# Kernel optimization log

Measured on AMD Instinct MI355X. Metric: run time of the kernel, lower is better.

Reference implementation:

```python
import jax, jax.numpy as jnp
import numpy as np
import math

B, S, D, H = 2, 2048, 1024, 16
DH = D // H  # head_dim = 64


def setup_inputs() -> dict:
    key = jax.random.key(0)
    k0, k1, k2 = jax.random.split(key, 3)
    x = jax.random.normal(k0, (B, S, D), dtype=jnp.float32)
    Wi = jax.random.normal(k1, (3 * D, D), dtype=jnp.float32) * 0.02  # torch (out,in) layout
    bi = jnp.zeros((3 * D,), dtype=jnp.float32)
    Wo = jax.random.normal(k2, (D, D), dtype=jnp.float32) * 0.02
    bo = jnp.zeros((D,), dtype=jnp.float32)
    return {"x": x, "Wi": Wi, "bi": bi, "Wo": Wo, "bo": bo, "causal_mask": 1}


def reference(x, Wi, bi, Wo, bo, causal_mask):
    b, s, d = x.shape
    # fused QKV projection: nn.Linear applies x @ W.T + b
    qkv = x @ Wi.T + bi                      # (b, s, 3d)
    q, k, v = jnp.split(qkv, 3, axis=-1)
    # (b, s, d) -> (b, h, s, dh)
    def to_heads(t):
        return t.reshape(b, s, H, DH).transpose(0, 2, 1, 3)
    q, k, v = to_heads(q), to_heads(k), to_heads(v)
    scores = jnp.einsum("bhqd,bhkd->bhqk", q, k)  # (b, h, s, s)
    if causal_mask:
        # mask strictly-upper triangle with -inf BEFORE scaling (as in source; -inf unaffected)
        tri = jnp.triu(jnp.ones((s, s), dtype=bool), k=1)
        scores = jnp.where(tri, -jnp.inf, scores)
    scores = scores / math.sqrt(DH)
    weight = jax.nn.softmax(scores, axis=-1)
    out = jnp.einsum("bhqk,bhkd->bhqd", weight, v)  # (b, h, s, dh)
    out = out.transpose(0, 2, 1, 3).reshape(b, s, d)
    return out @ Wo.T + bo
```

## Files before the change

kernel.cpp:

```cpp
#include <hip/hip_runtime.h>
#include <hip/hip_bf16.h>
#include <stdint.h>

#define B_    2
#define S_    2048
#define D_    1024
#define H_    16
#define DH_   64
#define MTOT  (B_*S_)
#define NQKV  (3*D_)

typedef __attribute__((ext_vector_type(8))) short  bf16x8;
typedef __attribute__((ext_vector_type(4))) short  bf16x4;
typedef __attribute__((ext_vector_type(4))) float  f32x4;
typedef __attribute__((ext_vector_type(8))) unsigned short u16x8;
typedef unsigned short ushort_t;

__device__ __forceinline__ ushort_t f2bf(float f) {
  union { float f; unsigned int i; } v; v.f = f;
  unsigned int r = v.i + 0x7FFF + ((v.i >> 16) & 1);
  return (ushort_t)(r >> 16);
}

__device__ __forceinline__ unsigned cvt_pk_bf16(float lo, float hi) {
  unsigned r;
  asm("v_cvt_pk_bf16_f32 %0, %1, %2" : "=v"(r) : "v"(lo), "v"(hi));
  return r;
}

__device__ __forceinline__ float fexp2(float x) {
  float r;
  asm("v_exp_f32 %0, %1" : "=v"(r) : "v"(x));
  return r;
}

#if __has_builtin(__builtin_amdgcn_mfma_f32_16x16x16_bf16)
__device__ __forceinline__ f32x4 mfma16(bf16x4 a, bf16x4 b, f32x4 c) {
  return __builtin_amdgcn_mfma_f32_16x16x16_bf16(a, b, c, 0, 0, 0);
}
#elif __has_builtin(__builtin_amdgcn_mfma_f32_16x16x16bf16_1k)
__device__ __forceinline__ f32x4 mfma16(bf16x4 a, bf16x4 b, f32x4 c) {
  return __builtin_amdgcn_mfma_f32_16x16x16bf16_1k(a, b, c, 0, 0, 0);
}
#else
__device__ __forceinline__ f32x4 mfma16(bf16x4 a, bf16x4 b, f32x4 c) {
  asm volatile("v_mfma_f32_16x16x16_bf16 %0, %1, %2, %0"
               : "+v"(c) : "v"(a), "v"(b));
  return c;
}
#endif

__device__ __forceinline__ void gl_lds16(const ushort_t* g, ushort_t* l) {
  __builtin_amdgcn_global_load_lds(
      (const __attribute__((address_space(1))) unsigned int*)g,
      (__attribute__((address_space(3))) unsigned int*)l, 16, 0, 0);
}

#define CVN1 (MTOT*D_/8)
#define CVN2 (NQKV*D_/8)
#define CVN3 (D_*D_/8)
__global__ __launch_bounds__(256) void cvt_all(
    const float* __restrict__ x, const float* __restrict__ Wi, const float* __restrict__ Wo,
    ushort_t* __restrict__ xb, ushort_t* __restrict__ Wib, ushort_t* __restrict__ Wob) {
  int i = blockIdx.x * blockDim.x + threadIdx.x;
  const float* src; ushort_t* dst; int k;
  if (i < CVN1)            { src = x;  dst = xb;  k = i; }
  else if (i < CVN1+CVN2)  { src = Wi; dst = Wib; k = i - CVN1; }
  else                     { src = Wo; dst = Wob; k = i - CVN1 - CVN2; }
  const float4* s4 = (const float4*)src;
  float4 a = s4[2*k], b = s4[2*k+1];
  u16x8 o;
  o[0]=f2bf(a.x); o[1]=f2bf(a.y); o[2]=f2bf(a.z); o[3]=f2bf(a.w);
  o[4]=f2bf(b.x); o[5]=f2bf(b.y); o[6]=f2bf(b.z); o[7]=f2bf(b.w);
  ((u16x8*)dst)[k] = o;
}

#define BKg 32
#define QSCALE 0.18033688011112042f
__global__ __launch_bounds__(256) void gemm_qkv(
    const ushort_t* __restrict__ Abf, const ushort_t* __restrict__ Bbf,
    const float* __restrict__ bias,
    ushort_t* __restrict__ qb, ushort_t* __restrict__ kb, ushort_t* __restrict__ vb) {
  __shared__ __align__(16) ushort_t Al[2][128*BKg];
  __shared__ __align__(16) ushort_t Bl[2][128*BKg];
  int tid = threadIdx.x;
  int w = tid >> 6, lane = tid & 63;
  int wrow = (w >> 1) * 64, wcol = (w & 1) * 64;
  int m0 = blockIdx.y * 128, n0 = blockIdx.x * 128;
  const int K = D_;
  const int nt = K / BKg;

  auto stageg = [&](int t, int buf) {
    int k0 = t * BKg;
    #pragma unroll
    for (int it = 0; it < 2; ++it) {
      int c = it*256 + tid;
      int row = c >> 2, cc = c & 3;
      int lbase = (it*256 + w*64) * 8;
      gl_lds16(Abf + (size_t)(m0+row)*K + k0 + cc*8, &Al[buf][lbase]);
      gl_lds16(Bbf + (size_t)(n0+row)*K + k0 + cc*8, &Bl[buf][lbase]);
    }
  };

  f32x4 zero = {0.f, 0.f, 0.f, 0.f};
  f32x4 acc[4][4];
  for (int i=0;i<4;i++) for (int j=0;j<4;j++) acc[i][j] = zero;

  stageg(0, 0);
  __syncthreads();

  for (int t = 0; t < nt; ++t) {
    int cur = t & 1;
    if (t + 1 < nt) stageg(t + 1, cur ^ 1);
    int kof = (lane >> 4) * 8;
    bf16x8 af[4], bfr[4];
    for (int i=0;i<4;i++) af[i]  = *(const bf16x8*)(&Al[cur][(wrow + i*16 + (lane&15))*BKg + kof]);
    for (int j=0;j<4;j++) bfr[j] = *(const bf16x8*)(&Bl[cur][(wcol + j*16 + (lane&15))*BKg + kof]);
    for (int i=0;i<4;i++)
      for (int j=0;j<4;j++)
        acc[i][j] = __builtin_amdgcn_mfma_f32_16x16x32_bf16(af[i], bfr[j], acc[i][j], 0, 0, 0);
    __syncthreads();
  }
  for (int i=0;i<4;i++)
    for (int j=0;j<4;j++)
      for (int r=0;r<4;r++) {
        int gm = m0 + wrow + i*16 + (lane>>4)*4 + r;
        int gn = n0 + wcol + j*16 + (lane&15);
        float v = acc[i][j][r] + bias[gn];
        int b = gm >> 11, s = gm & (S_-1);
        int sect = gn >> 10, hn = gn & (D_-1);
        int hh = hn >> 6, d = hn & 63;
        size_t idx = (((size_t)(b*H_ + hh))*S_ + s)*DH_ + d;
        if (sect == 0) v *= QSCALE;
        ushort_t val = f2bf(v);
        if (sect == 0) qb[idx] = val;
        else if (sect == 1) kb[idx] = val;
        else vb[idx] = val;
      }
}

__global__ __launch_bounds__(256) void transpose_v(
    const ushort_t* __restrict__ vb, ushort_t* __restrict__ vtb) {
  __shared__ ushort_t T[64*72];
  int bh = blockIdx.y;
  int s0 = blockIdx.x * 64;
  int tid = threadIdx.x;
  const ushort_t* src = vb + (size_t)bh * S_ * DH_;
  ushort_t* dst = vtb + (size_t)bh * DH_ * S_;
  for (int it = 0; it < 2; ++it) {
    int c = it*256 + tid;
    int row = c >> 3, cc = c & 7;
    *(uint4*)&T[row*72 + cc*8] = *(const uint4*)(src + (size_t)(s0+row)*DH_ + cc*8);
  }
  __syncthreads();
  for (int it = 0; it < 2; ++it) {
    int c = it*256 + tid;
    int d = c >> 3, sc = c & 7;
    u16x8 o;
    #pragma unroll
    for (int e = 0; e < 8; ++e) o[e] = T[(sc*8+e)*72 + d];
    *(u16x8*)(dst + (size_t)d*S_ + s0 + sc*8) = o;
  }
}

#define KVB 64
#define DTHR 8.0f
__global__ __launch_bounds__(256) void attn_fwd(
    const ushort_t* __restrict__ qb, const ushort_t* __restrict__ kb,
    const ushort_t* __restrict__ vtb, ushort_t* __restrict__ attnb,
    const int* __restrict__ causal) {
  int wg = blockIdx.x;
  int xcd = wg & 7;
  int rest = wg >> 3;
  int bh = (rest & 3) * 8 + xcd;
  int qblk = 31 - (rest >> 2);
  int b = bh >> 4, h = bh & 15;
  int tid = threadIdx.x, w = tid >> 6, lane = tid & 63;
  int g = lane >> 4, q16 = lane & 15;
  const ushort_t* qh  = qb  + (size_t)bh * S_ * DH_;
  const ushort_t* kh  = kb  + (size_t)bh * S_ * DH_;
  const ushort_t* vth = vtb + (size_t)bh * DH_ * S_;
  __shared__ __align__(16) ushort_t Kl[3][KVB*64];
  __shared__ __align__(16) ushort_t Vtl[3][64*KVB];
  bool use_causal = (causal[0] != 0);

  int nkv = use_causal ? (qblk + 1) : (S_/KVB);
  int qw = qblk*64 + w*16;

  bf16x8 qc0 = *(const bf16x8*)(qh + (size_t)(qw + q16)*DH_ +  0 + g*8);
  bf16x8 qc1 = *(const bf16x8*)(qh + (size_t)(qw + q16)*DH_ + 32 + g*8);

  int c0 = tid, c1 = tid + 256;
  int r0 = c0 >> 3, sw0 = ((c0 & 7) ^ (r0 & 7)) * 8;
  int r1 = c1 >> 3, sw1 = ((c1 & 7) ^ (r1 & 7)) * 8;
  const ushort_t* kp0 = kh + r0*DH_ + sw0;
  const ushort_t* kp1 = kh + r1*DH_ + sw1;
  const ushort_t* vp0 = vth + (size_t)r0*S_ + sw0;
  const ushort_t* vp1 = vth + (size_t)r1*S_ + sw1;

  auto stage = [&](int t, int buf) {
    size_t kadv = (size_t)(t*KVB) * DH_;
    int vadv = t*KVB;
    gl_lds16(kp0 + kadv, &Kl[buf][c0*8]);
    gl_lds16(kp1 + kadv, &Kl[buf][c1*8]);
    gl_lds16(vp0 + vadv, &Vtl[buf][c0*8]);
    gl_lds16(vp1 + vadv, &Vtl[buf][c1*8]);
  };

  f32x4 zero = {0.f,0.f,0.f,0.f};
  f32x4 o[4];
  #pragma unroll
  for (int dt=0;dt<4;dt++) o[dt] = zero;
  float mrun = -1e30f, lrun = 0.f;

  stage(0, 0);
  stage(1, 1);
  asm volatile("s_waitcnt vmcnt(4)" ::: "memory");
  __builtin_amdgcn_s_barrier();

  for (int it = 0; it < nkv; ++it) {
    int cur = it % 3;
    int kvbase = it * KVB;
    if (it + 2 < nkv) stage(it + 2, (it + 2) % 3);

    f32x4 sacc[4];
    #pragma unroll
    for (int j=0;j<4;j++) sacc[j] = zero;
    #pragma unroll
    for (int kk=0;kk<2;kk++) {
      bf16x8 qf = kk ? qc1 : qc0;
      #pragma unroll
      for (int j=0;j<4;j++) {
        int row = j*16 + q16;
        int slot = (kk*4 + g) ^ (row & 7);
        bf16x8 kf = *(const bf16x8*)(&Kl[cur][row*64 + slot*8]);
        sacc[j] = __builtin_amdgcn_mfma_f32_16x16x32_bf16(kf, qf, sacc[j], 0, 0, 0);
      }
    }
    if (use_causal && kvbase + KVB - 1 > qw) {
      int qd = qw + q16 - kvbase;
      #pragma unroll
      for (int j=0;j<4;j++)
        #pragma unroll
        for (int r=0;r<4;r++)
          if (16*j + 4*g + r > qd) sacc[j][r] = -1e30f;
    }
    float m0v = fmaxf(fmaxf(sacc[0][0], sacc[0][1]), fmaxf(sacc[0][2], sacc[0][3]));
    float m1v = fmaxf(fmaxf(sacc[1][0], sacc[1][1]), fmaxf(sacc[1][2], sacc[1][3]));
    float m2v = fmaxf(fmaxf(sacc[2][0], sacc[2][1]), fmaxf(sacc[2][2], sacc[2][3]));
    float m3v = fmaxf(fmaxf(sacc[3][0], sacc[3][1]), fmaxf(sacc[3][2], sacc[3][3]));
    float mx = fmaxf(fmaxf(m0v, m1v), fmaxf(m2v, m3v));
    mx = fmaxf(mx, __shfl_xor(mx, 16, 64));
    mx = fmaxf(mx, __shfl_xor(mx, 32, 64));
    if (!__all(mx - mrun <= DTHR)) {
      float mnew = fmaxf(mrun, mx);
      float alpha = fexp2(mrun - mnew);
      lrun *= alpha;
      float av0 = __shfl(alpha, 4*g + 0, 64);
      float av1 = __shfl(alpha, 4*g + 1, 64);
      float av2 = __shfl(alpha, 4*g + 2, 64);
      float av3 = __shfl(alpha, 4*g + 3, 64);
      #pragma unroll
      for (int dt=0;dt<4;dt++) {
        o[dt][0] *= av0; o[dt][1] *= av1; o[dt][2] *= av2; o[dt][3] *= av3;
      }
      mrun = mnew;
    }
    float p[4][4];
    float rs = 0.f;
    #pragma unroll
    for (int j=0;j<4;j++)
      #pragma unroll
      for (int r=0;r<4;r++) {
        p[j][r] = fexp2(sacc[j][r] - mrun);
        rs += p[j][r];
      }
    rs += __shfl_xor(rs, 16, 64);
    rs += __shfl_xor(rs, 32, 64);
    lrun += rs;
    #pragma unroll
    for (int s=0;s<4;s++) {
      union { unsigned u[2]; bf16x4 v; } pk;
      pk.u[0] = cvt_pk_bf16(p[s][0], p[s][1]);
      pk.u[1] = cvt_pk_bf16(p[s][2], p[s][3]);
      int E = 16*s + 4*g;
      #pragma unroll
      for (int dt=0;dt<4;dt++) {
        int row = dt*16 + q16;
        int off = row*64 + ((E >> 3) ^ (row & 7))*8 + (E & 7);
        bf16x4 vf = *(const bf16x4*)(&Vtl[cur][off]);
        o[dt] = mfma16(pk.v, vf, o[dt]);
      }
    }
    if (it + 2 < nkv) {
      asm volatile("s_waitcnt vmcnt(4)" ::: "memory");
    } else {
      asm volatile("s_waitcnt vmcnt(0)" ::: "memory");
    }
    __builtin_amdgcn_s_barrier();
  }
  float li0 = 1.f / __shfl(lrun, 4*g + 0, 64);
  float li1 = 1.f / __shfl(lrun, 4*g + 1, 64);
  float li2 = 1.f / __shfl(lrun, 4*g + 2, 64);
  float li3 = 1.f / __shfl(lrun, 4*g + 3, 64);
  #pragma unroll
  for (int r=0;r<4;r++) {
    float li = (r==0)?li0:(r==1)?li1:(r==2)?li2:li3;
    int q = qw + 4*g + r;
    #pragma unroll
    for (int dt=0;dt<4;dt++) {
      int d = dt*16 + q16;
      attnb[((size_t)(b*S_ + q))*D_ + h*DH_ + d] = f2bf(o[dt][r] * li);
    }
  }
}

__global__ __launch_bounds__(256) void gemm_out(
    const ushort_t* __restrict__ Abf, const ushort_t* __restrict__ Bbf,
    const float* __restrict__ bias, float* __restrict__ out) {
  __shared__ __align__(16) ushort_t Al[2][128*BKg];
  __shared__ __align__(16) ushort_t Bl[2][128*BKg];
  int tid = threadIdx.x;
  int w = tid >> 6, lane = tid & 63;
  int wrow = (w >> 1) * 64, wcol = (w & 1) * 64;
  int m0 = blockIdx.y * 128, n0 = blockIdx.x * 128;
  const int K = D_;
  const int nt = K / BKg;

  auto stageg = [&](int t, int buf) {
    int k0 = t * BKg;
    #pragma unroll
    for (int it = 0; it < 2; ++it) {
      int c = it*256 + tid;
      int row = c >> 2, cc = c & 3;
      int lbase = (it*256 + w*64) * 8;
      gl_lds16(Abf + (size_t)(m0+row)*K + k0 + cc*8, &Al[buf][lbase]);
      gl_lds16(Bbf + (size_t)(n0+row)*K + k0 + cc*8, &Bl[buf][lbase]);
    }
  };

  f32x4 zero = {0.f,0.f,0.f,0.f};
  f32x4 acc[4][4];
  for (int i=0;i<4;i++) for (int j=0;j<4;j++) acc[i][j] = zero;

  stageg(0, 0);
  __syncthreads();

  for (int t = 0; t < nt; ++t) {
    int cur = t & 1;
    if (t + 1 < nt) stageg(t + 1, cur ^ 1);
    int kof = (lane >> 4) * 8;
    bf16x8 af[4], bfr[4];
    for (int i=0;i<4;i++) af[i]  = *(const bf16x8*)(&Al[cur][(wrow + i*16 + (lane&15))*BKg + kof]);
    for (int j=0;j<4;j++) bfr[j] = *(const bf16x8*)(&Bl[cur][(wcol + j*16 + (lane&15))*BKg + kof]);
    for (int i=0;i<4;i++)
      for (int j=0;j<4;j++)
        acc[i][j] = __builtin_amdgcn_mfma_f32_16x16x32_bf16(af[i], bfr[j], acc[i][j], 0, 0, 0);
    __syncthreads();
  }
  for (int i=0;i<4;i++)
    for (int j=0;j<4;j++)
      for (int r=0;r<4;r++) {
        int gm = m0 + wrow + i*16 + (lane>>4)*4 + r;
        int gn = n0 + wcol + j*16 + (lane&15);
        out[(size_t)gm*D_ + gn] = acc[i][j][r] + bias[gn];
      }
}

extern "C" void kernel_launch(void* const* d_in, const int* in_sizes, int n_in,
                              void* d_out, int out_size, void* d_ws, size_t ws_size,
                              hipStream_t stream) {
  const float* x  = (const float*)d_in[0];
  const float* Wi = (const float*)d_in[1];
  const float* bi = (const float*)d_in[2];
  const float* Wo = (const float*)d_in[3];
  const float* bo = (const float*)d_in[4];
  const int* causal = (const int*)d_in[5];
  float* out = (float*)d_out;

  ushort_t* xb   = (ushort_t*)d_ws;
  ushort_t* Wib  = xb  + (size_t)MTOT*D_;
  ushort_t* Wob  = Wib + (size_t)NQKV*D_;
  ushort_t* qbuf = Wob + (size_t)D_*D_;
  ushort_t* kbuf = qbuf + (size_t)B_*H_*S_*DH_;
  ushort_t* vbuf = kbuf + (size_t)B_*H_*S_*DH_;
  ushort_t* attnb = vbuf + (size_t)B_*H_*S_*DH_;
  ushort_t* vtb  = xb;

  int ntot = CVN1 + CVN2 + CVN3;
  cvt_all<<<(ntot+255)/256, 256, 0, stream>>>(x, Wi, Wo, xb, Wib, Wob);

  gemm_qkv<<<dim3(NQKV/128, MTOT/128), 256, 0, stream>>>(xb, Wib, bi, qbuf, kbuf, vbuf);
  transpose_v<<<dim3(S_/64, B_*H_), 256, 0, stream>>>(vbuf, vtb);
  attn_fwd<<<1024, 256, 0, stream>>>(qbuf, kbuf, vtb, attnb, causal);
  gemm_out<<<dim3(D_/128, MTOT/128), 256, 0, stream>>>(attnb, Wob, bo, out);
}
```

Baseline: 130.9 us.

## Single-buffer GEMMs, widen output GEMM to 512 threads, add MFMA priority hints

```diff
diff --git a/kernel.cpp b/kernel.cpp
--- a/kernel.cpp
+++ b/kernel.cpp
@@ -75,51 +75,42 @@
   ((u16x8*)dst)[k] = o;
 }
 
-#define BKg 32
+#define BKQ 32
+#define BKO 64
 #define QSCALE 0.18033688011112042f
 __global__ __launch_bounds__(256) void gemm_qkv(
     const ushort_t* __restrict__ Abf, const ushort_t* __restrict__ Bbf,
     const float* __restrict__ bias,
     ushort_t* __restrict__ qb, ushort_t* __restrict__ kb, ushort_t* __restrict__ vb) {
-  __shared__ __align__(16) ushort_t Al[2][128*BKg];
-  __shared__ __align__(16) ushort_t Bl[2][128*BKg];
+  __shared__ __align__(16) ushort_t Al[128*BKQ];
+  __shared__ __align__(16) ushort_t Bl[128*BKQ];
   int tid = threadIdx.x;
   int w = tid >> 6, lane = tid & 63;
   int wrow = (w >> 1) * 64, wcol = (w & 1) * 64;
   int m0 = blockIdx.y * 128, n0 = blockIdx.x * 128;
   const int K = D_;
-  const int nt = K / BKg;
-
-  auto stageg = [&](int t, int buf) {
-    int k0 = t * BKg;
-    #pragma unroll
+  f32x4 zero = {0.f, 0.f, 0.f, 0.f};
+  f32x4 acc[4][4];
+  for (int i=0;i<4;i++) for (int j=0;j<4;j++) acc[i][j] = zero;
+
+  for (int k0 = 0; k0 < K; k0 += BKQ) {
+    __syncthreads();
     for (int it = 0; it < 2; ++it) {
       int c = it*256 + tid;
       int row = c >> 2, cc = c & 3;
       int lbase = (it*256 + w*64) * 8;
-      gl_lds16(Abf + (size_t)(m0+row)*K + k0 + cc*8, &Al[buf][lbase]);
-      gl_lds16(Bbf + (size_t)(n0+row)*K + k0 + cc*8, &Bl[buf][lbase]);
-    }
-  };
-
-  f32x4 zero = {0.f, 0.f, 0.f, 0.f};
-  f32x4 acc[4][4];
-  for (int i=0;i<4;i++) for (int j=0;j<4;j++) acc[i][j] = zero;
-
-  stageg(0, 0);
-  __syncthreads();
-
-  for (int t = 0; t < nt; ++t) {
-    int cur = t & 1;
-    if (t + 1 < nt) stageg(t + 1, cur ^ 1);
+      gl_lds16(Abf + (size_t)(m0+row)*K + k0 + cc*8, Al + lbase);
+      gl_lds16(Bbf + (size_t)(n0+row)*K + k0 + cc*8, Bl + lbase);
+    }
+    asm volatile("s_waitcnt vmcnt(0)" ::: "memory");
+    __syncthreads();
     int kof = (lane >> 4) * 8;
     bf16x8 af[4], bfr[4];
-    for (int i=0;i<4;i++) af[i]  = *(const bf16x8*)(&Al[cur][(wrow + i*16 + (lane&15))*BKg + kof]);
-    for (int j=0;j<4;j++) bfr[j] = *(const bf16x8*)(&Bl[cur][(wcol + j*16 + (lane&15))*BKg + kof]);
+    for (int i=0;i<4;i++) af[i]  = *(const bf16x8*)(Al + (wrow + i*16 + (lane&15))*BKQ + kof);
+    for (int j=0;j<4;j++) bfr[j] = *(const bf16x8*)(Bl + (wcol + j*16 + (lane&15))*BKQ + kof);
     for (int i=0;i<4;i++)
       for (int j=0;j<4;j++)
         acc[i][j] = __builtin_amdgcn_mfma_f32_16x16x32_bf16(af[i], bfr[j], acc[i][j], 0, 0, 0);
-    __syncthreads();
   }
   for (int i=0;i<4;i++)
     for (int j=0;j<4;j++)
@@ -226,6 +217,7 @@
     f32x4 sacc[4];
     #pragma unroll
     for (int j=0;j<4;j++) sacc[j] = zero;
+    __builtin_amdgcn_s_setprio(1);
     #pragma unroll
     for (int kk=0;kk<2;kk++) {
       bf16x8 qf = kk ? qc1 : qc0;
@@ -237,6 +229,7 @@
         sacc[j] = __builtin_amdgcn_mfma_f32_16x16x32_bf16(kf, qf, sacc[j], 0, 0, 0);
       }
     }
+    __builtin_amdgcn_s_setprio(0);
     if (use_causal && kvbase + KVB - 1 > qw) {
       int qd = qw + q16 - kvbase;
       #pragma unroll
@@ -278,6 +271,7 @@
     rs += __shfl_xor(rs, 16, 64);
     rs += __shfl_xor(rs, 32, 64);
     lrun += rs;
+    __builtin_amdgcn_s_setprio(1);
     #pragma unroll
     for (int s=0;s<4;s++) {
       union { unsigned u[2]; bf16x4 v; } pk;
@@ -292,6 +286,7 @@
         o[dt] = mfma16(pk.v, vf, o[dt]);
       }
     }
+    __builtin_amdgcn_s_setprio(0);
     if (it + 2 < nkv) {
       asm volatile("s_waitcnt vmcnt(4)" ::: "memory");
     } else {
@@ -315,54 +310,62 @@
   }
 }
 
-__global__ __launch_bounds__(256) void gemm_out(
+__global__ __launch_bounds__(512) void gemm_out(
     const ushort_t* __restrict__ Abf, const ushort_t* __restrict__ Bbf,
     const float* __restrict__ bias, float* __restrict__ out) {
-  __shared__ __align__(16) ushort_t Al[2][128*BKg];
-  __shared__ __align__(16) ushort_t Bl[2][128*BKg];
+  __shared__ __align__(16) ushort_t Al[128*BKO];
+  __shared__ __align__(16) ushort_t Bl[128*BKO];
   int tid = threadIdx.x;
   int w = tid >> 6, lane = tid & 63;
-  int wrow = (w >> 1) * 64, wcol = (w & 1) * 64;
+  int g = lane >> 4, q16 = lane & 15;
+  int wrow = (w >> 2) * 64, wcol = (w & 3) * 32;
   int m0 = blockIdx.y * 128, n0 = blockIdx.x * 128;
   const int K = D_;
-  const int nt = K / BKg;
-
-  auto stageg = [&](int t, int buf) {
-    int k0 = t * BKg;
+  f32x4 zero = {0.f,0.f,0.f,0.f};
+  f32x4 acc[4][2];
+  for (int i=0;i<4;i++) for (int j=0;j<2;j++) acc[i][j] = zero;
+
+  for (int k0 = 0; k0 < K; k0 += BKO) {
+    __syncthreads();
     #pragma unroll
     for (int it = 0; it < 2; ++it) {
-      int c = it*256 + tid;
-      int row = c >> 2, cc = c & 3;
-      int lbase = (it*256 + w*64) * 8;
-      gl_lds16(Abf + (size_t)(m0+row)*K + k0 + cc*8, &Al[buf][lbase]);
-      gl_lds16(Bbf + (size_t)(n0+row)*K + k0 + cc*8, &Bl[buf][lbase]);
-    }
-  };
-
-  f32x4 zero = {0.f,0.f,0.f,0.f};
-  f32x4 acc[4][4];
-  for (int i=0;i<4;i++) for (int j=0;j<4;j++) acc[i][j] = zero;
-
-  stageg(0, 0);
-  __syncthreads();
-
-  for (int t = 0; t < nt; ++t) {
-    int cur = t & 1;
-    if (t + 1 < nt) stageg(t + 1, cur ^ 1);
-    int kof = (lane >> 4) * 8;
-    bf16x8 af[4], bfr[4];
-    for (int i=0;i<4;i++) af[i]  = *(const bf16x8*)(&Al[cur][(wrow + i*16 + (lane&15))*BKg + kof]);
-    for (int j=0;j<4;j++) bfr[j] = *(const bf16x8*)(&Bl[cur][(wcol + j*16 + (lane&15))*BKg + kof]);
-    for (int i=0;i<4;i++)
-      for (int j=0;j<4;j++)
-        acc[i][j] = __builtin_amdgcn_mfma_f32_16x16x32_bf16(af[i], bfr[j], acc[i][j], 0, 0, 0);
+      int c = it*512 + tid;
+      int row = c >> 3, scc = ((c & 7) ^ (row & 7)) * 8;
+      gl_lds16(Abf + (size_t)(m0+row)*K + k0 + scc, Al + c*8);
+      gl_lds16(Bbf + (size_t)(n0+row)*K + k0 + scc, Bl + c*8);
+    }
+    asm volatile("s_waitcnt vmcnt(0)" ::: "memory");
     __syncthreads();
-  }
+    #pragma unroll
+    for (int kk = 0; kk < 2; ++kk) {
+      bf16x8 af[4], bfr[2];
+      #pragma unroll
+      for (int i=0;i<4;i++) {
+        int row = wrow + i*16 + q16;
+        int slot = ((kk*4 + g) ^ (row & 7)) * 8;
+        af[i] = *(const bf16x8*)(Al + row*BKO + slot);
+      }
+      #pragma unroll
+      for (int j=0;j<2;j++) {
+        int row = wcol + j*16 + q16;
+        int slot = ((kk*4 + g) ^ (row & 7)) * 8;
+        bfr[j] = *(const bf16x8*)(Bl + row*BKO + slot);
+      }
+      #pragma unroll
+      for (int i=0;i<4;i++)
+        #pragma unroll
+        for (int j=0;j<2;j++)
+          acc[i][j] = __builtin_amdgcn_mfma_f32_16x16x32_bf16(af[i], bfr[j], acc[i][j], 0, 0, 0);
+    }
+  }
+  #pragma unroll
   for (int i=0;i<4;i++)
-    for (int j=0;j<4;j++)
+    #pragma unroll
+    for (int j=0;j<2;j++)
+      #pragma unroll
       for (int r=0;r<4;r++) {
-        int gm = m0 + wrow + i*16 + (lane>>4)*4 + r;
-        int gn = n0 + wcol + j*16 + (lane&15);
+        int gm = m0 + wrow + i*16 + g*4 + r;
+        int gn = n0 + wcol + j*16 + q16;
         out[(size_t)gm*D_ + gn] = acc[i][j][r] + bias[gn];
       }
 }
@@ -393,5 +396,5 @@
   gemm_qkv<<<dim3(NQKV/128, MTOT/128), 256, 0, stream>>>(xb, Wib, bi, qbuf, kbuf, vbuf);
   transpose_v<<<dim3(S_/64, B_*H_), 256, 0, stream>>>(vbuf, vtb);
   attn_fwd<<<1024, 256, 0, stream>>>(qbuf, kbuf, vtb, attnb, causal);
-  gemm_out<<<dim3(D_/128, MTOT/128), 256, 0, stream>>>(attnb, Wob, bo, out);
-}
+  gemm_out<<<dim3(D_/128, MTOT/128), 512, 0, stream>>>(attnb, Wob, bo, out);
+}
```

New measurement: 122.4 us. 1.07x faster.
